# Optimization experiments

Measured on AMD Instinct MI355X. Metric: run time of the kernel, lower is better.

The kernel has to match this reference:

```python
import jax, jax.numpy as jnp
import numpy as np

T, IN, H, OUT = 8192, 9, 1024, 1


def setup_inputs() -> dict:
    key = jax.random.key(0)
    ks = jax.random.split(key, 11)
    s = 1.0 / np.sqrt(H)  # PyTorch LSTM/Linear init range

    def u(k, shape):
        return jax.random.uniform(k, shape, jnp.float32, -s, s)

    return {
        "input_seq": jax.random.normal(ks[0], (T, IN), jnp.float32),
        "w_ih0": u(ks[1], (4 * H, IN)), "w_hh0": u(ks[2], (4 * H, H)),
        "b_ih0": u(ks[3], (4 * H,)), "b_hh0": u(ks[4], (4 * H,)),
        "w_ih1": u(ks[5], (4 * H, H)), "w_hh1": u(ks[6], (4 * H, H)),
        "b_ih1": u(ks[7], (4 * H,)), "b_hh1": u(ks[8], (4 * H,)),
        "w_lin": u(ks[9], (OUT, H)), "b_lin": u(ks[10], (OUT,)),
    }


def _lstm_layer(xs, w_ih, w_hh, b_ih, b_hh):
    # xs: [T, in]. Precompute input contribution to gates for all timesteps.
    gx = xs @ w_ih.T + (b_ih + b_hh)  # [T, 4H]
    h_dim = w_hh.shape[1]

    def step(carry, g_x):
        h, c = carry
        g = g_x + h @ w_hh.T  # [4H], PyTorch gate order i,f,g,o
        i, f, gg, o = jnp.split(g, 4)
        i = jax.nn.sigmoid(i)
        f = jax.nn.sigmoid(f)
        gg = jnp.tanh(gg)
        o = jax.nn.sigmoid(o)
        c = f * c + i * gg
        h = o * jnp.tanh(c)
        return (h, c), h

    init = (jnp.zeros((h_dim,), xs.dtype), jnp.zeros((h_dim,), xs.dtype))
    _, hs = jax.lax.scan(step, init, gx)
    return hs  # [T, H]


def reference(input_seq, w_ih0, w_hh0, b_ih0, b_hh0,
              w_ih1, w_hh1, b_ih1, b_hh1, w_lin, b_lin):
    h1 = _lstm_layer(input_seq, w_ih0, w_hh0, b_ih0, b_hh0)  # layer 0
    h2 = _lstm_layer(h1, w_ih1, w_hh1, b_ih1, b_hh1)          # layer 1 (eval: no dropout)
    # predictions[-1] == Linear(lstm_out[-1])
    return h2[-1] @ w_lin.T + b_lin  # [OUT]
```

## Files before the change

### kernel.cpp

```cpp
#include <hip/hip_runtime.h>
#include <stdint.h>


#define TSTEPS 8192
#define HDIM   1024
#define BS     512
#define NBLK   256
#define RINGM  3

typedef unsigned long long u64;
typedef unsigned int u32;

__device__ __forceinline__ float sigm(float x)  { return 1.0f / (1.0f + __expf(-x)); }
__device__ __forceinline__ float tanh_(float x) { return 1.0f - 2.0f / (__expf(2.0f * x) + 1.0f); }
__device__ __forceinline__ float dot4(float4 a, float4 b) {
  return a.x * b.x + a.y * b.y + a.z * b.z + a.w * b.w;
}
__device__ __forceinline__ void pin4(float4& v) {
  asm volatile("" : "+v"(v.x), "+v"(v.y), "+v"(v.z), "+v"(v.w));
}

__device__ __forceinline__ u64 pollslot(const u64* p, u32 want) {
  u64 v = __hip_atomic_load(p, __ATOMIC_RELAXED, __HIP_MEMORY_SCOPE_AGENT);
  while ((u32)(v >> 32) != want) {
    __builtin_amdgcn_s_sleep(1);
    v = __hip_atomic_load(p, __ATOMIC_RELAXED, __HIP_MEMORY_SCOPE_AGENT);
  }
  return v;
}

__device__ __forceinline__ void publish(u64* p, u32 seq, float h) {
  u64 v = ((u64)seq << 32) | (u64)__float_as_uint(h);
  __hip_atomic_store(p, v, __ATOMIC_RELAXED, __HIP_MEMORY_SCOPE_AGENT);
}

__global__ void
__launch_bounds__(BS)
__attribute__((amdgpu_waves_per_eu(2, 2)))
lstm_fused(
    const float* __restrict__ xin,
    const float* __restrict__ wih0,
    const float* __restrict__ whh0,
    const float* __restrict__ bih0, const float* __restrict__ bhh0,
    const float* __restrict__ wih1,
    const float* __restrict__ whh1,
    const float* __restrict__ bih1, const float* __restrict__ bhh1,
    const float* __restrict__ wlin, const float* __restrict__ blin,
    float* __restrict__ out,
    u64* __restrict__ pub1, u64* __restrict__ pub2)
{
  const int b   = blockIdx.x;
  const int tid = threadIdx.x;
  const int wv  = tid >> 6;
  const int ln  = tid & 63;
  const bool isL0 = (wv < 4);
  const int unit = 4 * b + (wv & 3);

  __shared__ __align__(16) float hA[HDIM];
  __shared__ __align__(16) float hB[HDIM];
  __shared__ float red8[8];

  float4 wrr[4][4];
  {
    const float* WR = isL0 ? whh0 : whh1;
    #pragma unroll
    for (int g = 0; g < 4; ++g)
      #pragma unroll
      for (int j = 0; j < 4; ++j) {
        wrr[g][j] = *reinterpret_cast<const float4*>(
            WR + (size_t)(g * HDIM + unit) * HDIM + 4 * ln + 256 * j);
        pin4(wrr[g][j]);
      }
  }
  float4 wii[4][4];
  if (!isL0) {
    #pragma unroll
    for (int g = 0; g < 4; ++g)
      #pragma unroll
      for (int j = 0; j < 4; ++j) {
        wii[g][j] = *reinterpret_cast<const float4*>(
            wih1 + (size_t)(g * HDIM + unit) * HDIM + 4 * ln + 256 * j);
        pin4(wii[g][j]);
      }
  }
  float wxr[4][9];
  if (isL0) {
    #pragma unroll
    for (int g = 0; g < 4; ++g) {
      #pragma unroll
      for (int k = 0; k < 9; ++k)
        wxr[g][k] = wih0[(size_t)(g * HDIM + unit) * 9 + k];
      asm volatile("" : "+v"(wxr[g][0]), "+v"(wxr[g][1]), "+v"(wxr[g][2]),
                        "+v"(wxr[g][3]), "+v"(wxr[g][4]), "+v"(wxr[g][5]),
                        "+v"(wxr[g][6]), "+v"(wxr[g][7]), "+v"(wxr[g][8]));
    }
  }
  float bias[4];
  #pragma unroll
  for (int g = 0; g < 4; ++g)
    bias[g] = isL0 ? (bih0[g * HDIM + unit] + bhh0[g * HDIM + unit])
                   : (bih1[g * HDIM + unit] + bhh1[g * HDIM + unit]);
  asm volatile("" : "+v"(bias[0]), "+v"(bias[1]), "+v"(bias[2]), "+v"(bias[3]));

  float c = 0.0f;

  for (int r = 0; r <= TSTEPS; ++r) {
    float xr[9];
    if (isL0 && r < TSTEPS) {
      #pragma unroll
      for (int k = 0; k < 9; ++k) xr[k] = xin[r * 9 + k];
    }

    const int i2 = tid * 2;
    if (r >= 1) {
      const u64* s1 = pub1 + (size_t)((r - 1) & RINGM) * HDIM;
      u64 va = pollslot(s1 + i2, (u32)r);
      u64 vb = pollslot(s1 + i2 + 1, (u32)r);
      hA[i2]     = __uint_as_float((u32)va);
      hA[i2 + 1] = __uint_as_float((u32)vb);
    } else {
      hA[i2] = 0.0f; hA[i2 + 1] = 0.0f;
    }
    if (r >= 2) {
      const u64* s2 = pub2 + (size_t)((r - 2) & RINGM) * HDIM;
      u64 va = pollslot(s2 + i2, (u32)(r - 1));
      u64 vb = pollslot(s2 + i2 + 1, (u32)(r - 1));
      hB[i2]     = __uint_as_float((u32)va);
      hB[i2 + 1] = __uint_as_float((u32)vb);
    } else {
      hB[i2] = 0.0f; hB[i2 + 1] = 0.0f;
    }
    __syncthreads();

    if (isL0) {
      if (r < TSTEPS) {
        float a0 = 0, a1 = 0, a2 = 0, a3 = 0;
        #pragma unroll
        for (int j = 0; j < 4; ++j) {
          float4 h4 = reinterpret_cast<const float4*>(hA)[ln + (j << 6)];
          a0 += dot4(wrr[0][j], h4); a1 += dot4(wrr[1][j], h4);
          a2 += dot4(wrr[2][j], h4); a3 += dot4(wrr[3][j], h4);
        }
        #pragma unroll
        for (int d = 1; d < 64; d <<= 1) {
          a0 += __shfl_xor(a0, d); a1 += __shfl_xor(a1, d);
          a2 += __shfl_xor(a2, d); a3 += __shfl_xor(a3, d);
        }
        float g0 = a0 + bias[0], g1 = a1 + bias[1];
        float g2 = a2 + bias[2], g3 = a3 + bias[3];
        #pragma unroll
        for (int k = 0; k < 9; ++k) {
          g0 += wxr[0][k] * xr[k]; g1 += wxr[1][k] * xr[k];
          g2 += wxr[2][k] * xr[k]; g3 += wxr[3][k] * xr[k];
        }
        float gi = sigm(g0), gf = sigm(g1), gg = tanh_(g2), go = sigm(g3);
        c = gf * c + gi * gg;
        float h = go * tanh_(c);
        if (ln == 0)
          publish(pub1 + (size_t)(r & RINGM) * HDIM + unit, (u32)(r + 1), h);
      }
    } else {
      if (r >= 1) {
        float a0 = 0, a1 = 0, a2 = 0, a3 = 0;
        #pragma unroll
        for (int j = 0; j < 4; ++j) {
          float4 ha = reinterpret_cast<const float4*>(hA)[ln + (j << 6)];
          float4 hb = reinterpret_cast<const float4*>(hB)[ln + (j << 6)];
          a0 += dot4(wii[0][j], ha) + dot4(wrr[0][j], hb);
          a1 += dot4(wii[1][j], ha) + dot4(wrr[1][j], hb);
          a2 += dot4(wii[2][j], ha) + dot4(wrr[2][j], hb);
          a3 += dot4(wii[3][j], ha) + dot4(wrr[3][j], hb);
        }
        #pragma unroll
        for (int d = 1; d < 64; d <<= 1) {
          a0 += __shfl_xor(a0, d); a1 += __shfl_xor(a1, d);
          a2 += __shfl_xor(a2, d); a3 += __shfl_xor(a3, d);
        }
        float g0 = a0 + bias[0], g1 = a1 + bias[1];
        float g2 = a2 + bias[2], g3 = a3 + bias[3];
        float gi = sigm(g0), gf = sigm(g1), gg = tanh_(g2), go = sigm(g3);
        c = gf * c + gi * gg;
        float h = go * tanh_(c);
        if (ln == 0)
          publish(pub2 + (size_t)((r - 1) & RINGM) * HDIM + unit, (u32)r, h);
      }
    }
    __syncthreads();
  }

  if (b == 0) {
    const u64* s2 = pub2 + (size_t)((TSTEPS - 1) & RINGM) * HDIM;
    const int i2 = tid * 2;
    u64 va = pollslot(s2 + i2, (u32)TSTEPS);
    u64 vb = pollslot(s2 + i2 + 1, (u32)TSTEPS);
    float p = __uint_as_float((u32)va) * wlin[i2]
            + __uint_as_float((u32)vb) * wlin[i2 + 1];
    #pragma unroll
    for (int d = 1; d < 64; d <<= 1) p += __shfl_xor(p, d);
    if (ln == 0) red8[wv] = p;
    __syncthreads();
    if (tid == 0) {
      float s = blin[0];
      #pragma unroll
      for (int w = 0; w < 8; ++w) s += red8[w];
      out[0] = s;
    }
  }
}

extern "C" void kernel_launch(void* const* d_in, const int* in_sizes, int n_in,
                              void* d_out, int out_size, void* d_ws, size_t ws_size,
                              hipStream_t stream)
{
  const float* xin  = (const float*)d_in[0];
  const float* wih0 = (const float*)d_in[1];
  const float* whh0 = (const float*)d_in[2];
  const float* bih0 = (const float*)d_in[3];
  const float* bhh0 = (const float*)d_in[4];
  const float* wih1 = (const float*)d_in[5];
  const float* whh1 = (const float*)d_in[6];
  const float* bih1 = (const float*)d_in[7];
  const float* bhh1 = (const float*)d_in[8];
  const float* wlin = (const float*)d_in[9];
  const float* blin = (const float*)d_in[10];
  float* out = (float*)d_out;

  u64* pub1 = (u64*)d_ws;
  u64* pub2 = pub1 + 4 * HDIM;

  void* args[] = { &xin, &wih0, &whh0, &bih0, &bhh0,
                   &wih1, &whh1, &bih1, &bhh1, &wlin, &blin,
                   &out, &pub1, &pub2 };
  hipLaunchCooperativeKernel(reinterpret_cast<void*>(&lstm_fused),
                             dim3(NBLK), dim3(BS), args, 0, stream);
}
```

Baseline: 19.38 ms.

## Add per-XCD mirror of published hidden states to cut cross-die polling

Blocks are grouped by XCC ID, and the blocks in each group cooperatively copy the global published h vectors into a mirror buffer for that XCD. They use 16-byte cache-coherent loads for this copy. Other blocks then poll the mirror through L2 and fall back to direct polling after a timeout. Shared h buffers are double-buffered so the trailing __syncthreads per step can be dropped, and the poll sleep is lengthened. This aims to cut cross-die coherence traffic and one barrier per step, but it adds an extra hop of latency and a fallback path that is fragile.

Measured after the change: 27.99 ms. +44.5%, slower.

```diff
diff --git a/kernel.cpp b/kernel.cpp
--- a/kernel.cpp
+++ b/kernel.cpp
@@ -1,5 +1,8 @@
 #include <hip/hip_runtime.h>
+#include <hip/hip_cooperative_groups.h>
 #include <stdint.h>
+
+namespace cg = cooperative_groups;
 
 
 #define TSTEPS 8192
@@ -10,6 +13,7 @@
 
 typedef unsigned long long u64;
 typedef unsigned int u32;
+typedef __attribute__((ext_vector_type(4))) unsigned int u32x4;
 
 __device__ __forceinline__ float sigm(float x)  { return 1.0f / (1.0f + __expf(-x)); }
 __device__ __forceinline__ float tanh_(float x) { return 1.0f - 2.0f / (__expf(2.0f * x) + 1.0f); }
@@ -20,10 +24,26 @@
   asm volatile("" : "+v"(v.x), "+v"(v.y), "+v"(v.z), "+v"(v.w));
 }
 
+__device__ __forceinline__ void ld16cc(u32x4& r, const u64* p) {
+  asm volatile("global_load_dwordx4 %0, %1, off sc0 sc1" : "=&v"(r) : "v"(p));
+}
+__device__ __forceinline__ void ld16l2(u32x4& r, const u64* p) {
+  asm volatile("global_load_dwordx4 %0, %1, off sc0" : "=&v"(r) : "v"(p));
+}
+__device__ __forceinline__ void st16(u64* p, u32x4 v) {
+  asm volatile("global_store_dwordx4 %0, %1, off" :: "v"(p), "v"(v) : "memory");
+}
+__device__ __forceinline__ void wait1(u32x4& a) {
+  asm volatile("s_waitcnt vmcnt(0)" : "+v"(a) :: "memory");
+}
+__device__ __forceinline__ void wait2(u32x4& a, u32x4& b) {
+  asm volatile("s_waitcnt vmcnt(0)" : "+v"(a), "+v"(b) :: "memory");
+}
+
 __device__ __forceinline__ u64 pollslot(const u64* p, u32 want) {
   u64 v = __hip_atomic_load(p, __ATOMIC_RELAXED, __HIP_MEMORY_SCOPE_AGENT);
   while ((u32)(v >> 32) != want) {
-    __builtin_amdgcn_s_sleep(1);
+    __builtin_amdgcn_s_sleep(2);
     v = __hip_atomic_load(p, __ATOMIC_RELAXED, __HIP_MEMORY_SCOPE_AGENT);
   }
   return v;
@@ -47,7 +67,9 @@
     const float* __restrict__ bih1, const float* __restrict__ bhh1,
     const float* __restrict__ wlin, const float* __restrict__ blin,
     float* __restrict__ out,
-    u64* __restrict__ pub1, u64* __restrict__ pub2)
+    u64* __restrict__ pub1, u64* __restrict__ pub2,
+    u64* __restrict__ mir,
+    u32* __restrict__ cnt)
 {
   const int b   = blockIdx.x;
   const int tid = threadIdx.x;
@@ -56,9 +78,23 @@
   const bool isL0 = (wv < 4);
   const int unit = 4 * b + (wv & 3);
 
-  __shared__ __align__(16) float hA[HDIM];
-  __shared__ __align__(16) float hB[HDIM];
+  __shared__ __align__(16) float hA[2][HDIM];
+  __shared__ __align__(16) float hB[2][HDIM];
   __shared__ float red8[8];
+  __shared__ u32 sh_xr[2];
+  __shared__ int useDir;
+
+  if (tid == 0) {
+    u32 x;
+    asm volatile("s_getreg_b32 %0, hwreg(HW_REG_XCC_ID)" : "=s"(x));
+    x &= 7;
+    sh_xr[0] = x;
+    sh_xr[1] = atomicAdd(&cnt[x], 1u);
+    useDir = 0;
+  }
+  __syncthreads();
+  const u32 xcd = sh_xr[0];
+  const u32 rank = sh_xr[1];
 
   float4 wrr[4][4];
   {
@@ -102,6 +138,11 @@
                    : (bih1[g * HDIM + unit] + bhh1[g * HDIM + unit]);
   asm volatile("" : "+v"(bias[0]), "+v"(bias[1]), "+v"(bias[2]), "+v"(bias[3]));
 
+  cg::this_grid().sync();
+  const u32 nloc = __hip_atomic_load(&cnt[xcd], __ATOMIC_RELAXED,
+                                     __HIP_MEMORY_SCOPE_AGENT);
+  u64* mirx = mir + (size_t)xcd * (4 * 2048);
+
   float c = 0.0f;
 
   for (int r = 0; r <= TSTEPS; ++r) {
@@ -112,32 +153,86 @@
     }
 
     const int i2 = tid * 2;
-    if (r >= 1) {
-      const u64* s1 = pub1 + (size_t)((r - 1) & RINGM) * HDIM;
-      u64 va = pollslot(s1 + i2, (u32)r);
-      u64 vb = pollslot(s1 + i2 + 1, (u32)r);
-      hA[i2]     = __uint_as_float((u32)va);
-      hA[i2 + 1] = __uint_as_float((u32)vb);
+    float* hAr = hA[r & 1];
+    float* hBr = hB[r & 1];
+
+    if (r == 0) {
+      hA[0][i2] = 0.0f; hA[0][i2 + 1] = 0.0f;
+      hB[0][i2] = 0.0f; hB[0][i2 + 1] = 0.0f;
+      hB[1][i2] = 0.0f; hB[1][i2 + 1] = 0.0f;
     } else {
-      hA[i2] = 0.0f; hA[i2 + 1] = 0.0f;
-    }
-    if (r >= 2) {
-      const u64* s2 = pub2 + (size_t)((r - 2) & RINGM) * HDIM;
-      u64 va = pollslot(s2 + i2, (u32)(r - 1));
-      u64 vb = pollslot(s2 + i2 + 1, (u32)(r - 1));
-      hB[i2]     = __uint_as_float((u32)va);
-      hB[i2 + 1] = __uint_as_float((u32)vb);
-    } else {
-      hB[i2] = 0.0f; hB[i2 + 1] = 0.0f;
+      const u32 wA = (u32)r, wB = (u32)(r - 1);
+
+      if (wv == 0 && ln < 32) {
+        for (u32 s = rank; s < 32; s += nloc) {
+          if (r == 1 && s >= 16) break;
+          const u64* src; u32 want;
+          if (s < 16) {
+            src = pub1 + (size_t)((r - 1) & RINGM) * HDIM + s * 64 + 2 * ln;
+            want = wA;
+          } else {
+            src = pub2 + (size_t)((r - 2) & RINGM) * HDIM + (s - 16) * 64 + 2 * ln;
+            want = wB;
+          }
+          u32x4 v = {0, 0, 0, 0};
+          ld16cc(v, src); wait1(v);
+          while ((v.y != want) | (v.w != want)) {
+            __builtin_amdgcn_s_sleep(2);
+            ld16cc(v, src); wait1(v);
+          }
+          st16(mirx + (size_t)(r & RINGM) * 2048 + s * 64 + 2 * ln, v);
+        }
+      }
+
+      const u64* ma = mirx + (size_t)(r & RINGM) * 2048 + i2;
+      const u64* mb = ma + 1024;
+      const bool needB = (r >= 2);
+      bool okA = false, okB = !needB;
+      u32x4 va = {0, 0, 0, 0}, vb = {0, 0, 0, 0};
+      if (!*(volatile int*)&useDir) {
+        int it = 0;
+        ld16l2(va, ma);
+        if (needB) ld16l2(vb, mb);
+        wait2(va, vb);
+        for (;;) {
+          okA = (va.y == wA) & (va.w == wA);
+          if (needB) okB = (vb.y == wB) & (vb.w == wB);
+          if ((okA & okB) | (++it > 2000)) break;
+          __builtin_amdgcn_s_sleep(2);
+          if (!okA) ld16l2(va, ma);
+          if (needB && !okB) ld16l2(vb, mb);
+          wait2(va, vb);
+        }
+        if (!(okA & okB)) *(volatile int*)&useDir = 1;
+      }
+      if (!okA) {
+        const u64* p = pub1 + (size_t)((r - 1) & RINGM) * HDIM + i2;
+        va.x = (u32)pollslot(p, wA);
+        va.z = (u32)pollslot(p + 1, wA);
+      }
+      if (!okB) {
+        const u64* p = pub2 + (size_t)((r - 2) & RINGM) * HDIM + i2;
+        vb.x = (u32)pollslot(p, wB);
+        vb.z = (u32)pollslot(p + 1, wB);
+      }
+      hAr[i2]     = __uint_as_float(va.x);
+      hAr[i2 + 1] = __uint_as_float(va.z);
+      if (needB) {
+        hBr[i2]     = __uint_as_float(vb.x);
+        hBr[i2 + 1] = __uint_as_float(vb.z);
+      }
     }
     __syncthreads();
+
+    const float4* hA4 = reinterpret_cast<const float4*>(hAr);
+    const float4* hB4 = reinterpret_cast<const float4*>(hBr);
 
     if (isL0) {
       if (r < TSTEPS) {
         float a0 = 0, a1 = 0, a2 = 0, a3 = 0;
         #pragma unroll
         for (int j = 0; j < 4; ++j) {
-          float4 h4 = reinterpret_cast<const float4*>(hA)[ln + (j << 6)];
+          float4 h4 = hA4[ln + (j << 6)];
           a0 += dot4(wrr[0][j], h4); a1 += dot4(wrr[1][j], h4);
           a2 += dot4(wrr[2][j], h4); a3 += dot4(wrr[3][j], h4);
         }
@@ -164,8 +259,8 @@
         float a0 = 0, a1 = 0, a2 = 0, a3 = 0;
         #pragma unroll
         for (int j = 0; j < 4; ++j) {
-          float4 ha = reinterpret_cast<const float4*>(hA)[ln + (j << 6)];
-          float4 hb = reinterpret_cast<const float4*>(hB)[ln + (j << 6)];
+          float4 ha = hA4[ln + (j << 6)];
+          float4 hb = hB4[ln + (j << 6)];
           a0 += dot4(wii[0][j], ha) + dot4(wrr[0][j], hb);
           a1 += dot4(wii[1][j], ha) + dot4(wrr[1][j], hb);
           a2 += dot4(wii[2][j], ha) + dot4(wrr[2][j], hb);
@@ -185,7 +280,6 @@
           publish(pub2 + (size_t)((r - 1) & RINGM) * HDIM + unit, (u32)r, h);
       }
     }
-    __syncthreads();
   }
 
   if (b == 0) {
@@ -225,12 +319,17 @@
   const float* blin = (const float*)d_in[10];
   float* out = (float*)d_out;
 
-  u64* pub1 = (u64*)d_ws;
+  char* ws = (char*)d_ws;
+  u64* pub1 = (u64*)ws;
   u64* pub2 = pub1 + 4 * HDIM;
+  u32* cnt  = (u32*)(ws + 64 * 1024);
+  u64* mir  = (u64*)(ws + 65 * 1024);
+
+  hipMemsetAsync(cnt, 0, 8 * sizeof(u32), stream);
 
   void* args[] = { &xin, &wih0, &whh0, &bih0, &bhh0,
                    &wih1, &whh1, &bih1, &bhh1, &wlin, &blin,
-                   &out, &pub1, &pub2 };
+                   &out, &pub1, &pub2, &mir, &cnt };
   hipLaunchCooperativeKernel(reinterpret_cast<void*>(&lstm_fused),
                              dim3(NBLK), dim3(BS), args, 0, stream);
 }
```
